# Kernel tuning notes

Measured on AMD Instinct MI355X. Metric: run time of the kernel, lower is better.

Reference implementation:

```python
import math
import jax, jax.numpy as jnp
from jax import lax
import numpy as np

D = 256; H = 8; NL = 6; HALF = D // 2
B = 32; NEV = 256

def sinpos(x):
    # SinusoidalPosEmb: (..., ) int -> (..., D)
    freq = jnp.exp(jnp.arange(HALF, dtype=jnp.float32) * (-math.log(10000.0) / (HALF - 1)))
    e = x.astype(jnp.float32)[..., None] * freq
    return jnp.concatenate([jnp.sin(e), jnp.cos(e)], axis=-1)

def layer_norm(x, g, b, eps=1e-5):
    m = x.mean(-1, keepdims=True)
    v = ((x - m) ** 2).mean(-1, keepdims=True)
    return (x - m) / jnp.sqrt(v + eps) * g + b

def gelu(x):
    return jax.nn.gelu(x, approximate=False)

def conv1d(x, w, b, stride):
    y = lax.conv_general_dilated(x, w, (stride,), [(3, 3)], dimension_numbers=("NCH", "OIH", "NCH"))
    return y + b[None, :, None]

def setup_inputs():
    ks = iter(jax.random.split(jax.random.key(0), 48))
    def p(*shape):
        return jax.random.normal(next(ks), shape, dtype=jnp.float32) * 0.02
    inp = dict(
        mel=jax.random.normal(next(ks), (B, 80, 2000), dtype=jnp.float32),
        events=jnp.sort(jax.random.randint(next(ks), (B, NEV), 0, 2000), axis=-1),
        event_mask=jnp.zeros((B, NEV), dtype=bool),
        star_rating=jax.random.uniform(next(ks), (B,), dtype=jnp.float32) * 9.0,
        mel_W=p(16, 80), mel_b=p(16),
        conv1_w=p(128, 16, 7), conv1_b=p(128),
        gn_g=jnp.ones(128, jnp.float32), gn_b=jnp.zeros(128, jnp.float32),
        conv2_w=p(256, 128, 7), conv2_b=p(256),
        cn_g=jnp.ones(D, jnp.float32), cn_b=jnp.zeros(D, jnp.float32),
        star_table=p(20, D),
        ep_W1=p(D, 3 * D), ep_b1=p(D), ep_W2=p(D, D), ep_b2=p(D),
        tl_Wqkv=p(NL, 3 * D, D), tl_bqkv=p(NL, 3 * D),
        tl_Wo=p(NL, D, D), tl_bo=p(NL, D),
        tl_ln1g=jnp.ones((NL, D), jnp.float32), tl_ln1b=jnp.zeros((NL, D), jnp.float32),
        tl_ln2g=jnp.ones((NL, D), jnp.float32), tl_ln2b=jnp.zeros((NL, D), jnp.float32),
        tl_W1=p(NL, 4 * D, D), tl_b1=p(NL, 4 * D),
        tl_W2=p(NL, D, 4 * D), tl_b2=p(NL, D),
        pool_q=jax.random.normal(next(ks), (D,), dtype=jnp.float32),
        on_g=jnp.ones(D, jnp.float32), on_b=jnp.zeros(D, jnp.float32),
        oh_W=p(1, D), oh_b=p(1),
    )
    return inp

def reference(mel, events, event_mask, star_rating, mel_W, mel_b, conv1_w, conv1_b, gn_g, gn_b, conv2_w, conv2_b, cn_g, cn_b, star_table, ep_W1, ep_b1, ep_W2, ep_b2, tl_Wqkv, tl_bqkv, tl_Wo, tl_bo, tl_ln1g, tl_ln1b, tl_ln2g, tl_ln2b, tl_W1, tl_b1, tl_W2, tl_b2, pool_q, on_g, on_b, oh_W, oh_b):
    Bsz = mel.shape[0]
    # mel_compress on channel dim: (B,80,T) -> (B,16,T)
    x_mel = jnp.einsum('bct,oc->bot', mel, mel_W) + mel_b[None, :, None]
    h = gelu(conv1d(x_mel, conv1_w, conv1_b, 2))           # (B,128,1000)
    # GroupNorm(1, C): normalize over (C, L) per sample
    m = h.mean((1, 2), keepdims=True)
    v = ((h - m) ** 2).mean((1, 2), keepdims=True)
    h = (h - m) / jnp.sqrt(v + 1e-5) * gn_g[None, :, None] + gn_b[None, :, None]
    h = gelu(conv1d(h, conv2_w, conv2_b, 2))               # (B,256,500)
    x = h.transpose(0, 2, 1)                               # (B,500,256)
    x = layer_norm(x, cn_g, cn_b)
    S = x.shape[1]
    x = x + sinpos(jnp.arange(S))[None]
    star_bucket = jnp.clip((star_rating / 0.5).astype(jnp.int32), 0, star_table.shape[0] - 1)
    x = x + star_table[star_bucket][:, None, :]
    # --- event gap/ratio embeddings (vectorized; exact match to torch loop when all valid) ---
    diff = jnp.maximum(events[:, 1:] - events[:, :-1], 1)  # clamp(min=1)
    g = jnp.concatenate([diff[:, :1], diff], axis=1)        # g[0] = g[1]
    gap_ms = g * 5
    g_f = jnp.maximum(g.astype(jnp.float32), 1.0)
    r = jnp.clip(g_f[:, 1:] / g_f[:, :-1], 0.1, 10.0)
    ones = jnp.ones((Bsz, 1), dtype=jnp.float32)
    ratio_before = (jnp.concatenate([ones, r], axis=1) * 50).astype(jnp.int32)
    ratio_after = (jnp.concatenate([r, ones], axis=1) * 50).astype(jnp.int32)
    combined = jnp.concatenate([sinpos(ratio_before), sinpos(ratio_after), sinpos(gap_ms)], axis=-1)
    ev = gelu(combined @ ep_W1.T + ep_b1) @ ep_W2.T + ep_b2
    ev = jnp.where(event_mask[..., None], 0.0, ev)
    token_pos = jnp.clip(events // 4, 0, S - 1)
    # batched scatter-add of event embeddings into token stream
    x = x.at[jnp.arange(Bsz)[:, None], token_pos].add(ev)
    hd = D // H
    for i in range(NL):
        xn = layer_norm(x, tl_ln1g[i], tl_ln1b[i])
        qkv = xn @ tl_Wqkv[i].T + tl_bqkv[i]
        q, k, vv = jnp.split(qkv, 3, axis=-1)
        q = q.reshape(Bsz, S, H, hd).transpose(0, 2, 1, 3)
        k = k.reshape(Bsz, S, H, hd).transpose(0, 2, 1, 3)
        vv = vv.reshape(Bsz, S, H, hd).transpose(0, 2, 1, 3)
        a = jax.nn.softmax(jnp.einsum('bhqd,bhkd->bhqk', q, k) / math.sqrt(hd), axis=-1)
        o = jnp.einsum('bhqk,bhkd->bhqd', a, vv).transpose(0, 2, 1, 3).reshape(Bsz, S, D)
        x = x + o @ tl_Wo[i].T + tl_bo[i]
        xn = layer_norm(x, tl_ln2g[i], tl_ln2b[i])
        x = x + gelu(xn @ tl_W1[i].T + tl_b1[i]) @ tl_W2[i].T + tl_b2[i]
    # attention pooling + head
    logits = x @ pool_q / math.sqrt(D)
    w = jax.nn.softmax(logits, axis=-1)
    pooled = jnp.einsum('bs,bsd->bd', w, x)
    return (layer_norm(pooled, on_g, on_b) @ oh_W.T + oh_b).squeeze(-1)
```

## Files before the change

### kernel.cpp

```cpp
#include <hip/hip_runtime.h>
#include <math.h>

namespace {
constexpr int kB = 32;
constexpr int kS = 500;
constexpr int kH = 8;
}
#define LKC (-0.07252236513366287)

typedef __attribute__((ext_vector_type(8))) short s16x8;
typedef __attribute__((ext_vector_type(4))) float f32x4;

__device__ __forceinline__ float gelu_f(float x){
  return 0.5f * x * (1.0f + erff(x * 0.7071067811865476f));
}
__device__ __forceinline__ float b2f(short s){
  union { unsigned u; float f; } x; x.u = ((unsigned)(unsigned short)s) << 16; return x.f;
}
__device__ __forceinline__ short f2b(float f){
  unsigned u = __float_as_uint(f);
  unsigned r = (u + 0x7fffu + ((u >> 16) & 1u)) >> 16;
  return (short)r;
}

__global__ __launch_bounds__(256) void f2b_kernel(const float* __restrict__ in,
    short* __restrict__ out, int n){
  int i = blockIdx.x * 256 + threadIdx.x;
  if(i < n) out[i] = f2b(in[i]);
}
__global__ __launch_bounds__(128) void conv1w_pad(const float* __restrict__ w, short* __restrict__ out){
  int n = blockIdx.x, k = threadIdx.x;
  out[n*128 + k] = (k < 112) ? f2b(w[n*112 + k]) : (short)0;
}

template<int OUT, bool DOGELU>
__global__ __launch_bounds__(256) void gemm_mfma(const short* __restrict__ A,
    const short* __restrict__ W, const float* __restrict__ bias,
    void* __restrict__ Cv, int M, int N, int K){
  __shared__ __align__(16) short Al[128*64];
  __shared__ __align__(16) short Wl[128*64];
  const int t = threadIdx.x;
  const int wid = t >> 6, lane = t & 63;
  const int m0 = blockIdx.y * 128, n0 = blockIdx.x * 128;
  const int wr = (wid >> 1) * 64, wc = (wid & 1) * 64;
  const int frow = lane & 15, lg = lane >> 4;
  const int rA = t >> 3;
  const int sA = (t & 7) ^ (rA & 7);
  const short* Aq = A + (size_t)(m0 + rA) * K + sA * 8;
  const short* Wq = W + (size_t)(n0 + rA) * K + sA * 8;
  f32x4 acc[4][4] = {};
  for(int k0 = 0; k0 < K; k0 += 64){
    s16x8 av[4], wv[4];
    #pragma unroll
    for(int j = 0; j < 4; ++j){
      av[j] = *(const s16x8*)(Aq + k0 + (size_t)(32*j)*K);
      wv[j] = *(const s16x8*)(Wq + k0 + (size_t)(32*j)*K);
    }
    __syncthreads();
    #pragma unroll
    for(int j = 0; j < 4; ++j){
      *(s16x8*)&Al[t*8 + j*2048] = av[j];
      *(s16x8*)&Wl[t*8 + j*2048] = wv[j];
    }
    __syncthreads();
    #pragma unroll
    for(int kh = 0; kh < 2; ++kh){
      s16x8 a[4], b[4];
      #pragma unroll
      for(int mi = 0; mi < 4; ++mi){
        int r = wr + mi*16 + frow;
        a[mi] = *(const s16x8*)&Al[r*64 + (((kh*4 + lg) ^ (r & 7)) * 8)];
      }
      #pragma unroll
      for(int ni = 0; ni < 4; ++ni){
        int r = wc + ni*16 + frow;
        b[ni] = *(const s16x8*)&Wl[r*64 + (((kh*4 + lg) ^ (r & 7)) * 8)];
      }
      #pragma unroll
      for(int mi = 0; mi < 4; ++mi)
        #pragma unroll
        for(int ni = 0; ni < 4; ++ni)
          acc[mi][ni] = __builtin_amdgcn_mfma_f32_16x16x32_bf16(a[mi], b[ni], acc[mi][ni], 0, 0, 0);
    }
  }
  #pragma unroll
  for(int mi = 0; mi < 4; ++mi){
    #pragma unroll
    for(int ni = 0; ni < 4; ++ni){
      const int col = n0 + wc + ni*16 + (lane & 15);
      const float bv = bias[col];
      #pragma unroll
      for(int r = 0; r < 4; ++r){
        const int row = m0 + wr + mi*16 + (lane >> 4)*4 + r;
        float v = acc[mi][ni][r] + bv;
        if(DOGELU) v = gelu_f(v);
        if(OUT == 0) ((float*)Cv)[(size_t)row*N + col] = v;
        else if(OUT == 1) ((float*)Cv)[(size_t)row*N + col] += v;
        else ((short*)Cv)[(size_t)row*N + col] = f2b(v);
      }
    }
  }
}

template<bool DOGELU>
__global__ __launch_bounds__(512) void gemm512(const short* __restrict__ A,
    const short* __restrict__ W, const float* __restrict__ bias,
    short* __restrict__ C, int M, int N, int K){
  __shared__ __align__(16) short Al[64*64];
  __shared__ __align__(16) short Wl[256*64];
  const int t = threadIdx.x;
  const int wid = t >> 6, lane = t & 63;
  const int m0 = blockIdx.y * 64, n0 = blockIdx.x * 256;
  const int wm = wid >> 2, wn = wid & 3;
  const int frow = lane & 15, lg = lane >> 4;
  const int rA = t >> 3;
  const int sA = (t & 7) ^ (rA & 7);
  const short* Aq = A + (size_t)(m0 + rA) * K + sA * 8;
  const short* Wq = W + (size_t)(n0 + rA) * K + sA * 8;
  f32x4 acc[2][4] = {};
  for(int k0 = 0; k0 < K; k0 += 64){
    s16x8 av = *(const s16x8*)(Aq + k0);
    s16x8 wv[4];
    #pragma unroll
    for(int j = 0; j < 4; ++j)
      wv[j] = *(const s16x8*)(Wq + k0 + (size_t)(64*j)*K);
    __syncthreads();
    *(s16x8*)&Al[t*8] = av;
    #pragma unroll
    for(int j = 0; j < 4; ++j)
      *(s16x8*)&Wl[t*8 + j*4096] = wv[j];
    __syncthreads();
    #pragma unroll
    for(int kh = 0; kh < 2; ++kh){
      s16x8 a[2], b[4];
      #pragma unroll
      for(int mi = 0; mi < 2; ++mi){
        int r = wm*32 + mi*16 + frow;
        a[mi] = *(const s16x8*)&Al[r*64 + (((kh*4 + lg) ^ (r & 7)) * 8)];
      }
      #pragma unroll
      for(int ni = 0; ni < 4; ++ni){
        int r = wn*64 + ni*16 + frow;
        b[ni] = *(const s16x8*)&Wl[r*64 + (((kh*4 + lg) ^ (r & 7)) * 8)];
      }
      #pragma unroll
      for(int mi = 0; mi < 2; ++mi)
        #pragma unroll
        for(int ni = 0; ni < 4; ++ni)
          acc[mi][ni] = __builtin_amdgcn_mfma_f32_16x16x32_bf16(a[mi], b[ni], acc[mi][ni], 0, 0, 0);
    }
  }
  #pragma unroll
  for(int mi = 0; mi < 2; ++mi){
    #pragma unroll
    for(int ni = 0; ni < 4; ++ni){
      const int col = n0 + wn*64 + ni*16 + (lane & 15);
      const float bv = bias[col];
      #pragma unroll
      for(int r = 0; r < 4; ++r){
        const int row = m0 + wm*32 + mi*16 + (lane >> 4)*4 + r;
        float v = acc[mi][ni][r] + bv;
        if(DOGELU) v = gelu_f(v);
        C[(size_t)row*N + col] = f2b(v);
      }
    }
  }
}

template<bool DOLN>
__global__ __launch_bounds__(512) void gemm_ln(const short* __restrict__ A,
    const short* __restrict__ W, const float* __restrict__ bias,
    float* __restrict__ X, const float* __restrict__ lg_, const float* __restrict__ lb_,
    short* __restrict__ XNB, int M, int K){
  __shared__ __align__(16) short Al[64*64];
  __shared__ __align__(16) short Wl[256*64];
  __shared__ float sbuf[64][4];
  const int t = threadIdx.x;
  const int wid = t >> 6, lane = t & 63;
  const int m0 = blockIdx.y * 64;
  const int wm = wid >> 2, wn = wid & 3;
  const int frow = lane & 15, lg = lane >> 4;
  const int lq = lane & 15;
  const int rA = t >> 3;
  const int sA = (t & 7) ^ (rA & 7);
  const short* Aq = A + (size_t)(m0 + rA) * K + sA * 8;
  const short* Wq = W + (size_t)rA * K + sA * 8;
  f32x4 acc[2][4] = {};
  for(int k0 = 0; k0 < K; k0 += 64){
    s16x8 av = *(const s16x8*)(Aq + k0);
    s16x8 wv[4];
    #pragma unroll
    for(int j = 0; j < 4; ++j)
      wv[j] = *(const s16x8*)(Wq + k0 + (size_t)(64*j)*K);
    __syncthreads();
    *(s16x8*)&Al[t*8] = av;
    #pragma unroll
    for(int j = 0; j < 4; ++j)
      *(s16x8*)&Wl[t*8 + j*4096] = wv[j];
    __syncthreads();
    #pragma unroll
    for(int kh = 0; kh < 2; ++kh){
      s16x8 a[2], b[4];
      #pragma unroll
      for(int mi = 0; mi < 2; ++mi){
        int r = wm*32 + mi*16 + frow;
        a[mi] = *(const s16x8*)&Al[r*64 + (((kh*4 + lg) ^ (r & 7)) * 8)];
      }
      #pragma unroll
      for(int ni = 0; ni < 4; ++ni){
        int r = wn*64 + ni*16 + frow;
        b[ni] = *(const s16x8*)&Wl[r*64 + (((kh*4 + lg) ^ (r & 7)) * 8)];
      }
      #pragma unroll
      for(int mi = 0; mi < 2; ++mi)
        #pragma unroll
        for(int ni = 0; ni < 4; ++ni)
          acc[mi][ni] = __builtin_amdgcn_mfma_f32_16x16x32_bf16(a[mi], b[ni], acc[mi][ni], 0, 0, 0);
    }
  }
  float v[2][4][4];
  #pragma unroll
  for(int mi = 0; mi < 2; ++mi)
    #pragma unroll
    for(int ni = 0; ni < 4; ++ni){
      const int col = wn*64 + ni*16 + lq;
      const float bv = bias[col];
      #pragma unroll
      for(int r = 0; r < 4; ++r){
        const int row = m0 + wm*32 + mi*16 + lg*4 + r;
        v[mi][ni][r] = acc[mi][ni][r] + bv + X[(size_t)row*256 + col];
      }
    }
  __syncthreads();
  float vmean[2][4], vrstd[2][4];
  if(DOLN){
    #pragma unroll
    for(int mi = 0; mi < 2; ++mi)
      #pragma unroll
      for(int r = 0; r < 4; ++r){
        float s = v[mi][0][r] + v[mi][1][r] + v[mi][2][r] + v[mi][3][r];
        s += __shfl_xor(s, 1); s += __shfl_xor(s, 2);
        s += __shfl_xor(s, 4); s += __shfl_xor(s, 8);
        if(lq == 0) sbuf[wm*32 + mi*16 + lg*4 + r][wn] = s;
      }
    __syncthreads();
    #pragma unroll
    for(int mi = 0; mi < 2; ++mi)
      #pragma unroll
      for(int r = 0; r < 4; ++r){
        int rl = wm*32 + mi*16 + lg*4 + r;
        vmean[mi][r] = (sbuf[rl][0] + sbuf[rl][1] + sbuf[rl][2] + sbuf[rl][3]) * (1.f/256.f);
      }
    __syncthreads();
    #pragma unroll
    for(int mi = 0; mi < 2; ++mi)
      #pragma unroll
      for(int r = 0; r < 4; ++r){
        float q = 0.f;
        #pragma unroll
        for(int ni = 0; ni < 4; ++ni){ float d = v[mi][ni][r] - vmean[mi][r]; q += d*d; }
        q += __shfl_xor(q, 1); q += __shfl_xor(q, 2);
        q += __shfl_xor(q, 4); q += __shfl_xor(q, 8);
        if(lq == 0) sbuf[wm*32 + mi*16 + lg*4 + r][wn] = q;
      }
    __syncthreads();
    #pragma unroll
    for(int mi = 0; mi < 2; ++mi)
      #pragma unroll
      for(int r = 0; r < 4; ++r){
        int rl = wm*32 + mi*16 + lg*4 + r;
        float Q = sbuf[rl][0] + sbuf[rl][1] + sbuf[rl][2] + sbuf[rl][3];
        vrstd[mi][r] = 1.f / sqrtf(Q * (1.f/256.f) + 1e-5f);
      }
  }
  #pragma unroll
  for(int mi = 0; mi < 2; ++mi)
    #pragma unroll
    for(int ni = 0; ni < 4; ++ni){
      const int col = wn*64 + ni*16 + lq;
      float gg = 0.f, bb = 0.f;
      if(DOLN){ gg = lg_[col]; bb = lb_[col]; }
      #pragma unroll
      for(int r = 0; r < 4; ++r){
        const int row = m0 + wm*32 + mi*16 + lg*4 + r;
        float val = v[mi][ni][r];
        X[(size_t)row*256 + col] = val;
        if(DOLN)
          XNB[(size_t)row*256 + col] = f2b((val - vmean[mi][r]) * vrstd[mi][r] * gg + bb);
      }
    }
}

__global__ __launch_bounds__(256) void mel_kernel(const float* __restrict__ mel,
    const float* __restrict__ W, const float* __restrict__ bias, float* __restrict__ xm){
  __shared__ float Ws[16][80];
  __shared__ float bs[16];
  const int t = threadIdx.x;
  for(int i = t; i < 16*80; i += 256) Ws[i/80][i%80] = W[i];
  if(t < 16) bs[t] = bias[t];
  __syncthreads();
  int blk = blockIdx.x;
  int b = blk >> 3;
  int tc = (blk & 7) * 256 + t;
  if(tc >= 2000) return;
  float acc[16];
  #pragma unroll
  for(int o = 0; o < 16; ++o) acc[o] = bs[o];
  for(int c = 0; c < 80; ++c){
    float v = mel[((size_t)b*80 + c)*2000 + tc];
    #pragma unroll
    for(int o = 0; o < 16; ++o) acc[o] += v * Ws[o][c];
  }
  #pragma unroll
  for(int o = 0; o < 16; ++o) xm[((size_t)b*16 + o)*2000 + tc] = acc[o];
}

__global__ __launch_bounds__(256) void im2col1b(const float* __restrict__ xm, short* __restrict__ A){
  size_t idx = (size_t)blockIdx.x * 256 + threadIdx.x;
  int col = idx & 127;
  size_t row = idx >> 7;
  int t1 = row % 1000, b = row / 1000;
  float v = 0.f;
  if(col < 112){
    int i = col / 7, k = col % 7;
    int src = 2*t1 + k - 3;
    if(src >= 0 && src < 2000) v = xm[((size_t)b*16 + i)*2000 + src];
  }
  A[idx] = f2b(v);
}

__global__ __launch_bounds__(256) void gn_part(const float* __restrict__ h1, double* __restrict__ part){
  int blk = blockIdx.x;
  const float* p = h1 + (size_t)blk * 16000;
  int t = threadIdx.x;
  double s = 0, q = 0;
  for(int i = t; i < 16000; i += 256){ double v = p[i]; s += v; q += v*v; }
  __shared__ double rs[256], rq[256];
  rs[t] = s; rq[t] = q; __syncthreads();
  for(int s2 = 128; s2 > 0; s2 >>= 1){
    if(t < s2){ rs[t] += rs[t+s2]; rq[t] += rq[t+s2]; }
    __syncthreads();
  }
  if(t == 0){ part[blk*2] = rs[0]; part[blk*2+1] = rq[0]; }
}
__global__ __launch_bounds__(256) void gn_final(const double* __restrict__ part, float* __restrict__ stats){
  int t = threadIdx.x;
  int b = t >> 3;
  double s = part[t*2], q = part[t*2+1];
  s += __shfl_xor(s, 1); q += __shfl_xor(q, 1);
  s += __shfl_xor(s, 2); q += __shfl_xor(q, 2);
  s += __shfl_xor(s, 4); q += __shfl_xor(q, 4);
  if((t & 7) == 0){
    double mean = s / 128000.0;
    double var  = q / 128000.0 - mean*mean;
    stats[b*2]   = (float)mean;
    stats[b*2+1] = (float)(1.0 / sqrt(var + 1e-5));
  }
}

__global__ __launch_bounds__(256) void im2col2b(const float* __restrict__ h1,
    const float* __restrict__ stats, const float* __restrict__ gg,
    const float* __restrict__ gb, short* __restrict__ A){
  size_t idx = (size_t)blockIdx.x * 256 + threadIdx.x;
  int col = idx % 896;
  size_t row = idx / 896;
  int t2 = row % 500, b = row / 500;
  int i = col / 7, k = col % 7;
  int src = 2*t2 + k - 3;
  float v = 0.f;
  if(src >= 0 && src < 1000){
    float raw = h1[((size_t)b*1000 + src)*128 + i];
    v = (raw - stats[b*2]) * stats[b*2+1] * gg[i] + gb[i];
  }
  A[idx] = f2b(v);
}

__global__ __launch_bounds__(256) void postconv(const float* __restrict__ xp,
    const float* __restrict__ cg, const float* __restrict__ cb,
    const float* __restrict__ star, const float* __restrict__ stab,
    float* __restrict__ x){
  int row = blockIdx.x, t = threadIdx.x;
  int s = row % 500, b = row / 500;
  __shared__ float red[256];
  float v = xp[(size_t)row*256 + t];
  red[t] = v; __syncthreads();
  for(int s2 = 128; s2 > 0; s2 >>= 1){ if(t < s2) red[t] += red[t+s2]; __syncthreads(); }
  float mean = red[0] / 256.f; __syncthreads();
  float d = v - mean;
  red[t] = d*d; __syncthreads();
  for(int s2 = 128; s2 > 0; s2 >>= 1){ if(t < s2) red[t] += red[t+s2]; __syncthreads(); }
  float rstd = 1.f / sqrtf(red[0]/256.f + 1e-5f);
  int j = t & 127;
  double f = exp((double)j * LKC);
  double a = (double)s * f;
  float pe = (float)(t < 128 ? sin(a) : cos(a));
  int bucket = (int)(star[b] * 2.0f);
  bucket = bucket < 0 ? 0 : (bucket > 19 ? 19 : bucket);
  x[(size_t)row*256 + t] = d*rstd*cg[t] + cb[t] + pe + stab[bucket*256 + t];
}

__global__ __launch_bounds__(256) void event_feat(const int* __restrict__ events, short* __restrict__ comb){
  int blk = blockIdx.x;
  int e = blk & 255, b = blk >> 8;
  const int* ev = events + b*256;
  int t = threadIdx.x;
  auto gof = [&](int i){ int j = i < 1 ? 1 : i; int d = ev[j] - ev[j-1]; return d < 1 ? 1 : d; };
  int gi = gof(e);
  double rb = 1.0, ra = 1.0;
  if(e != 0){
    rb = (double)gi / (double)gof(e-1);
    rb = rb < 0.1 ? 0.1 : (rb > 10.0 ? 10.0 : rb);
  }
  if(e != 255){
    ra = (double)gof(e+1) / (double)gi;
    ra = ra < 0.1 ? 0.1 : (ra > 10.0 ? 10.0 : ra);
  }
  int rbi = (int)(rb * 50.0);
  int rai = (int)(ra * 50.0);
  int gap = 5 * gi;
  int j = t & 127;
  double f = exp((double)j * LKC);
  double a0 = (double)rbi * f, a1 = (double)rai * f, a2 = (double)gap * f;
  size_t base = (size_t)blk * 768;
  comb[base + t]       = f2b((float)(t < 128 ? sin(a0) : cos(a0)));
  comb[base + 256 + t] = f2b((float)(t < 128 ? sin(a1) : cos(a1)));
  comb[base + 512 + t] = f2b((float)(t < 128 ? sin(a2) : cos(a2)));
}

__global__ __launch_bounds__(256) void ev_scatter(const float* __restrict__ evout,
    const int* __restrict__ events, const unsigned char* __restrict__ mask,
    float* __restrict__ x){
  int blk = blockIdx.x;
  int e = blk & 255, b = blk >> 8;
  if(mask[b*256 + e]) return;
  int tp = events[b*256 + e] >> 2;
  tp = tp < 0 ? 0 : (tp > 499 ? 499 : tp);
  int t = threadIdx.x;
  atomicAdd(&x[((size_t)b*500 + tp)*256 + t], evout[(size_t)blk*256 + t]);
}

__global__ __launch_bounds__(256) void ln_rows(const float* __restrict__ x,
    const float* __restrict__ g, const float* __restrict__ b, short* __restrict__ out){
  int row = blockIdx.x, t = threadIdx.x;
  int wid = t >> 6, lane = t & 63;
  __shared__ float sm[8];
  float v = x[(size_t)row*256 + t];
  float s = v;
  #pragma unroll
  for(int o = 1; o < 64; o <<= 1) s += __shfl_xor(s, o);
  if(lane == 0) sm[wid] = s;
  __syncthreads();
  float mean = (sm[0] + sm[1] + sm[2] + sm[3]) * (1.f/256.f);
  float d = v - mean;
  float q = d*d;
  #pragma unroll
  for(int o = 1; o < 64; o <<= 1) q += __shfl_xor(q, o);
  if(lane == 0) sm[4 + wid] = q;
  __syncthreads();
  float rstd = 1.f / sqrtf((sm[4] + sm[5] + sm[6] + sm[7]) * (1.f/256.f) + 1e-5f);
  out[(size_t)row*256 + t] = f2b(d*rstd*g[t] + b[t]);
}

__global__ __launch_bounds__(512) void attn_mfma(const short* __restrict__ qkv,
    short* __restrict__ o){
  __shared__ __align__(16) short Kl[512*40];
  __shared__ __align__(16) short Vt[32*520];
  __shared__ __align__(16) short Pl[8][640];
  const int i = blockIdx.x;
  const int b = (i & 7)*4 + ((i >> 3) & 3);
  const int h = i >> 5;
  const int t = threadIdx.x;
  const int wid = t >> 6, lane = t & 63;
  const int lq = lane & 15, lg = lane >> 4;
  const short* base = qkv + (size_t)b * kS * 768;
  {
    const int c = t & 3;
    for(int idx = t; idx < 2048; idx += 512){
      int row = idx >> 2;
      s16x8 kv = {0,0,0,0,0,0,0,0};
      unsigned vu0 = 0, vu1 = 0, vu2 = 0, vu3 = 0;
      if(row < kS){
        const short* rp = base + (size_t)row*768 + 256 + h*32 + c*8;
        kv = *(const s16x8*)rp;
        uint4 vv = *(const uint4*)(rp + 256);
        vu0 = vv.x; vu1 = vv.y; vu2 = vv.z; vu3 = vv.w;
      }
      *(s16x8*)&Kl[row*40 + c*8] = kv;
      unsigned b0 = (c & 2) ? vu2 : vu0, b1 = (c & 2) ? vu3 : vu1;
      unsigned b2 = (c & 2) ? vu0 : vu2, b3 = (c & 2) ? vu1 : vu3;
      unsigned r0 = (c & 1) ? b1 : b0, r1 = (c & 1) ? b2 : b1;
      unsigned r2 = (c & 1) ? b3 : b2, r3 = (c & 1) ? b0 : b3;
      #pragma unroll
      for(int j0 = 0; j0 < 8; ++j0){
        unsigned w = (j0 >> 1) == 0 ? r0 : (j0 >> 1) == 1 ? r1 : (j0 >> 1) == 2 ? r2 : r3;
        short val = (short)((j0 & 1) ? (w >> 16) : (w & 0xffff));
        int d = c*8 + ((j0 + 2*c) & 7);
        Vt[d*520 + row] = val;
      }
    }
  }
  __syncthreads();
  const float scale = 0.17677669529663687f;
  short* pw = &Pl[wid][0];
  for(int qi = 0; qi < 4; ++qi){
    const int qt = wid*4 + qi;
    const int q0 = qt*16;
    int qrow = q0 + lq; if(qrow > kS-1) qrow = kS-1;
    s16x8 qf = *(const s16x8*)(base + (size_t)qrow*768 + h*32 + lg*8);
    f32x4 sc[32];
    __builtin_amdgcn_s_setprio(1);
    #pragma unroll
    for(int kt = 0; kt < 32; ++kt){
      s16x8 kf = *(const s16x8*)&Kl[(kt*16 + lq)*40 + lg*8];
      f32x4 z = {0.f,0.f,0.f,0.f};
      sc[kt] = __builtin_amdgcn_mfma_f32_16x16x32_bf16(kf, qf, z, 0, 0, 0);
    }
    __builtin_amdgcn_s_setprio(0);
    if(lg >= 1){ sc[31][0] = -1e30f; sc[31][1] = -1e30f; sc[31][2] = -1e30f; sc[31][3] = -1e30f; }
    float m = -1e30f;
    #pragma unroll
    for(int kt = 0; kt < 32; ++kt)
      m = fmaxf(m, fmaxf(fmaxf(sc[kt][0], sc[kt][1]), fmaxf(sc[kt][2], sc[kt][3])));
    m = fmaxf(m, __shfl_xor(m, 16, 64));
    m = fmaxf(m, __shfl_xor(m, 32, 64));
    float l = 0.f;
    #pragma unroll
    for(int kt = 0; kt < 32; ++kt){
      #pragma unroll
      for(int r = 0; r < 4; ++r){
        float p = expf((sc[kt][r] - m) * scale);
        sc[kt][r] = p;
        l += p;
      }
    }
    l += __shfl_xor(l, 16, 64);
    l += __shfl_xor(l, 32, 64);
    f32x4 oa0 = {0.f,0.f,0.f,0.f}, oa1 = {0.f,0.f,0.f,0.f};
    #pragma unroll
    for(int kt2 = 0; kt2 < 16; ++kt2){
      #pragma unroll
      for(int f = 0; f < 2; ++f){
        f32x4 p = sc[kt2*2 + f];
        uint2 pk;
        pk.x = (unsigned)(unsigned short)f2b(p[0]) | ((unsigned)(unsigned short)f2b(p[1]) << 16);
        pk.y = (unsigned)(unsigned short)f2b(p[2]) | ((unsigned)(unsigned short)f2b(p[3]) << 16);
        *(uint2*)&pw[lq*40 + f*16 + lg*4] = pk;
      }
      s16x8 pf = *(const s16x8*)&pw[lq*40 + lg*8];
      s16x8 v0 = *(const s16x8*)&Vt[lq*520 + kt2*32 + lg*8];
      s16x8 v1 = *(const s16x8*)&Vt[(16+lq)*520 + kt2*32 + lg*8];
      __builtin_amdgcn_s_setprio(1);
      oa0 = __builtin_amdgcn_mfma_f32_16x16x32_bf16(v0, pf, oa0, 0, 0, 0);
      oa1 = __builtin_amdgcn_mfma_f32_16x16x32_bf16(v1, pf, oa1, 0, 0, 0);
      __builtin_amdgcn_s_setprio(0);
    }
    float inv = 1.f / l;
    int qw = q0 + lq;
    if(qw < kS){
      short* op = o + ((size_t)(b*kS + qw))*256 + h*32;
      uint2 w0, w1;
      w0.x = (unsigned)(unsigned short)f2b(oa0[0]*inv) | ((unsigned)(unsigned short)f2b(oa0[1]*inv) << 16);
      w0.y = (unsigned)(unsigned short)f2b(oa0[2]*inv) | ((unsigned)(unsigned short)f2b(oa0[3]*inv) << 16);
      w1.x = (unsigned)(unsigned short)f2b(oa1[0]*inv) | ((unsigned)(unsigned short)f2b(oa1[1]*inv) << 16);
      w1.y = (unsigned)(unsigned short)f2b(oa1[2]*inv) | ((unsigned)(unsigned short)f2b(oa1[3]*inv) << 16);
      *(uint2*)&op[lg*4] = w0;
      *(uint2*)&op[16 + lg*4] = w1;
    }
  }
}

__global__ __launch_bounds__(256) void pool_head(const float* __restrict__ x,
    const float* __restrict__ pq, const float* __restrict__ og, const float* __restrict__ ob,
    const float* __restrict__ ohW, const float* __restrict__ ohb, float* __restrict__ out){
  int b = blockIdx.x, t = threadIdx.x;
  __shared__ float lg[500];
  __shared__ float red[256];
  const float* xb = x + (size_t)b * 500 * 256;
  for(int s = t; s < 500; s += 256){
    const float* xr = xb + (size_t)s * 256;
    float d = 0.f;
    for(int c = 0; c < 256; ++c) d += xr[c] * pq[c];
    lg[s] = d * 0.0625f;
  }
  __syncthreads();
  float m = -1e30f;
  for(int s = t; s < 500; s += 256) m = fmaxf(m, lg[s]);
  red[t] = m; __syncthreads();
  for(int s2 = 128; s2 > 0; s2 >>= 1){ if(t < s2) red[t] = fmaxf(red[t], red[t+s2]); __syncthreads(); }
  m = red[0]; __syncthreads();
  float ps = 0.f;
  for(int s = t; s < 500; s += 256){ float e = expf(lg[s] - m); lg[s] = e; ps += e; }
  red[t] = ps; __syncthreads();
  for(int s2 = 128; s2 > 0; s2 >>= 1){ if(t < s2) red[t] += red[t+s2]; __syncthreads(); }
  float inv = 1.f / red[0];
  __syncthreads();
  float acc = 0.f;
  for(int s = 0; s < 500; ++s) acc += lg[s] * xb[(size_t)s*256 + t];
  acc *= inv;
  __syncthreads();
  red[t] = acc; __syncthreads();
  for(int s2 = 128; s2 > 0; s2 >>= 1){ if(t < s2) red[t] += red[t+s2]; __syncthreads(); }
  float mean = red[0] / 256.f; __syncthreads();
  float d = acc - mean;
  red[t] = d*d; __syncthreads();
  for(int s2 = 128; s2 > 0; s2 >>= 1){ if(t < s2) red[t] += red[t+s2]; __syncthreads(); }
  float rstd = 1.f / sqrtf(red[0]/256.f + 1e-5f);
  __syncthreads();
  float val = (d*rstd*og[t] + ob[t]) * ohW[t];
  red[t] = val; __syncthreads();
  for(int s2 = 128; s2 > 0; s2 >>= 1){ if(t < s2) red[t] += red[t+s2]; __syncthreads(); }
  if(t == 0) out[b] = red[0] + ohb[0];
}

extern "C" void kernel_launch(void* const* d_in, const int* in_sizes, int n_in,
                              void* d_out, int out_size, void* d_ws, size_t ws_size,
                              hipStream_t stream){
  const float* mel      = (const float*)d_in[0];
  const int*   events   = (const int*)d_in[1];
  const unsigned char* emask = (const unsigned char*)d_in[2];
  const float* star     = (const float*)d_in[3];
  const float* mel_W    = (const float*)d_in[4];
  const float* mel_b    = (const float*)d_in[5];
  const float* conv1_w  = (const float*)d_in[6];
  const float* conv1_b  = (const float*)d_in[7];
  const float* gn_g     = (const float*)d_in[8];
  const float* gn_b     = (const float*)d_in[9];
  const float* conv2_w  = (const float*)d_in[10];
  const float* conv2_b  = (const float*)d_in[11];
  const float* cn_g     = (const float*)d_in[12];
  const float* cn_b     = (const float*)d_in[13];
  const float* star_tab = (const float*)d_in[14];
  const float* ep_W1    = (const float*)d_in[15];
  const float* ep_b1    = (const float*)d_in[16];
  const float* ep_W2    = (const float*)d_in[17];
  const float* ep_b2    = (const float*)d_in[18];
  const float* tl_Wqkv  = (const float*)d_in[19];
  const float* tl_bqkv  = (const float*)d_in[20];
  const float* tl_Wo    = (const float*)d_in[21];
  const float* tl_bo    = (const float*)d_in[22];
  const float* tl_ln1g  = (const float*)d_in[23];
  const float* tl_ln1b  = (const float*)d_in[24];
  const float* tl_ln2g  = (const float*)d_in[25];
  const float* tl_ln2b  = (const float*)d_in[26];
  const float* tl_W1    = (const float*)d_in[27];
  const float* tl_b1    = (const float*)d_in[28];
  const float* tl_W2    = (const float*)d_in[29];
  const float* tl_b2    = (const float*)d_in[30];
  const float* pool_q   = (const float*)d_in[31];
  const float* on_g     = (const float*)d_in[32];
  const float* on_b     = (const float*)d_in[33];
  const float* oh_W     = (const float*)d_in[34];
  const float* oh_b     = (const float*)d_in[35];
  (void)in_sizes; (void)n_in; (void)out_size; (void)ws_size;

  float* ws  = (float*)d_ws;
  float* X   = ws;
  short* XNB = (short*)(ws + 4096000);
  short* OB  = (short*)(ws + 6144000);
  short* WB  = (short*)(ws + 8192000);
  float* BIG = ws + 10812000;
  double* PART = (double*)(ws + 28668000);
  float* STATS = ws + 28671900;

  short* WBc1 = WB + 0;
  short* WBc2 = WB + 16384;
  short* WBe1 = WB + 245760;
  short* WBe2 = WB + 442368;
  short* WBqk = WB + 507904;
  short* WBwo = WB + 1687552;
  short* WBw1 = WB + 2080768;
  short* WBw2 = WB + 3653632;

  float* XMEL = BIG;
  short* A1B  = (short*)(BIG + 1024000);
  float* H1   = BIG + 3072000;
  short* A2B  = (short*)(BIG + 7168000);
  float* XPRE = BIG;
  short* COMBB= (short*)BIG;
  short* EHIDB= (short*)(BIG + 3146000);
  float* EVO  = BIG + 4195000;
  short* QKVB = (short*)BIG;
  short* HIDB = (short*)(BIG + 7168000);

  conv1w_pad<<<128, 128, 0, stream>>>(conv1_w, WBc1);
  f2b_kernel<<<896, 256, 0, stream>>>(conv2_w, WBc2, 229376);
  f2b_kernel<<<768, 256, 0, stream>>>(ep_W1, WBe1, 196608);
  f2b_kernel<<<256, 256, 0, stream>>>(ep_W2, WBe2, 65536);
  f2b_kernel<<<4608, 256, 0, stream>>>(tl_Wqkv, WBqk, 1179648);
  f2b_kernel<<<1536, 256, 0, stream>>>(tl_Wo, WBwo, 393216);
  f2b_kernel<<<6144, 256, 0, stream>>>(tl_W1, WBw1, 1572864);
  f2b_kernel<<<6144, 256, 0, stream>>>(tl_W2, WBw2, 1572864);

  mel_kernel<<<kB*8, 256, 0, stream>>>(mel, mel_W, mel_b, XMEL);
  im2col1b<<<16000, 256, 0, stream>>>(XMEL, A1B);
  gemm_mfma<0,true><<<dim3(1, 250), 256, 0, stream>>>(A1B, WBc1, conv1_b, H1, 32000, 128, 128);
  gn_part<<<256, 256, 0, stream>>>(H1, PART);
  gn_final<<<1, 256, 0, stream>>>(PART, STATS);
  im2col2b<<<56000, 256, 0, stream>>>(H1, STATS, gn_g, gn_b, A2B);
  gemm_mfma<0,true><<<dim3(2, 125), 256, 0, stream>>>(A2B, WBc2, conv2_b, XPRE, 16000, 256, 896);
  postconv<<<16000, 256, 0, stream>>>(XPRE, cn_g, cn_b, star, star_tab, X);
  event_feat<<<kB*256, 256, 0, stream>>>(events, COMBB);
  gemm_mfma<2,true><<<dim3(2, 64), 256, 0, stream>>>(COMBB, WBe1, ep_b1, EHIDB, 8192, 256, 768);
  gemm_mfma<0,false><<<dim3(2, 64), 256, 0, stream>>>(EHIDB, WBe2, ep_b2, EVO, 8192, 256, 256);
  ev_scatter<<<kB*256, 256, 0, stream>>>(EVO, events, emask, X);

  ln_rows<<<16000, 256, 0, stream>>>(X, tl_ln1g, tl_ln1b, XNB);
  for(int i = 0; i < 6; ++i){
    gemm512<false><<<dim3(3, 250), 512, 0, stream>>>(XNB, WBqk + (size_t)i*196608, tl_bqkv + i*768, QKVB, 16000, 768, 256);
    attn_mfma<<<kB*kH, 512, 0, stream>>>(QKVB, OB);
    gemm_ln<true><<<dim3(1, 250), 512, 0, stream>>>(OB, WBwo + (size_t)i*65536, tl_bo + i*256,
        X, tl_ln2g + i*256, tl_ln2b + i*256, XNB, 16000, 256);
    gemm512<true><<<dim3(4, 250), 512, 0, stream>>>(XNB, WBw1 + (size_t)i*262144, tl_b1 + i*1024, HIDB, 16000, 1024, 256);
    if(i < 5)
      gemm_ln<true><<<dim3(1, 250), 512, 0, stream>>>(HIDB, WBw2 + (size_t)i*262144, tl_b2 + i*256,
          X, tl_ln1g + (i+1)*256, tl_ln1b + (i+1)*256, XNB, 16000, 1024);
    else
      gemm_ln<false><<<dim3(1, 250), 512, 0, stream>>>(HIDB, WBw2 + (size_t)i*262144, tl_b2 + i*256,
          X, tl_ln1g, tl_ln1b, XNB, 16000, 1024);
  }

  pool_head<<<kB, 256, 0, stream>>>(X, pool_q, on_g, on_b, oh_W, oh_b, (float*)d_out);
}
```

Baseline: 995.0 us.

## Enlarge gemm512 M tile to 128 and drop max pass in attention softmax

The QKV and FFN1 GEMM now covers 128 rows per block instead of 64, doubling accumulators per wave to raise MFMA reuse of the weight tile and halve the grid. In attention, the softmax max-reduction is removed and exp2f with a folded scale is used, relying on small score magnitudes to avoid overflow. Manual bf16 rounding is replaced with the packed hardware convert instruction. The trade-offs are higher register pressure and fewer blocks in the GEMMs, plus a numerical-safety risk in the softmax if scores grow large.

```diff
diff --git a/kernel.cpp b/kernel.cpp
--- a/kernel.cpp
+++ b/kernel.cpp
@@ -21,6 +21,11 @@
   unsigned u = __float_as_uint(f);
   unsigned r = (u + 0x7fffu + ((u >> 16) & 1u)) >> 16;
   return (short)r;
+}
+__device__ __forceinline__ unsigned cvtpk(float lo, float hi){
+  unsigned r;
+  asm("v_cvt_pk_bf16_f32 %0, %1, %2" : "=v"(r) : "v"(lo), "v"(hi));
+  return r;
 }
 
 __global__ __launch_bounds__(256) void f2b_kernel(const float* __restrict__ in,
@@ -106,36 +111,38 @@
 __global__ __launch_bounds__(512) void gemm512(const short* __restrict__ A,
     const short* __restrict__ W, const float* __restrict__ bias,
     short* __restrict__ C, int M, int N, int K){
-  __shared__ __align__(16) short Al[64*64];
+  __shared__ __align__(16) short Al[128*64];
   __shared__ __align__(16) short Wl[256*64];
   const int t = threadIdx.x;
   const int wid = t >> 6, lane = t & 63;
-  const int m0 = blockIdx.y * 64, n0 = blockIdx.x * 256;
+  const int m0 = blockIdx.y * 128, n0 = blockIdx.x * 256;
   const int wm = wid >> 2, wn = wid & 3;
   const int frow = lane & 15, lg = lane >> 4;
   const int rA = t >> 3;
   const int sA = (t & 7) ^ (rA & 7);
   const short* Aq = A + (size_t)(m0 + rA) * K + sA * 8;
   const short* Wq = W + (size_t)(n0 + rA) * K + sA * 8;
-  f32x4 acc[2][4] = {};
+  f32x4 acc[4][4] = {};
   for(int k0 = 0; k0 < K; k0 += 64){
-    s16x8 av = *(const s16x8*)(Aq + k0);
-    s16x8 wv[4];
+    s16x8 av[2], wv[4];
+    av[0] = *(const s16x8*)(Aq + k0);
+    av[1] = *(const s16x8*)(Aq + k0 + (size_t)64*K);
     #pragma unroll
     for(int j = 0; j < 4; ++j)
       wv[j] = *(const s16x8*)(Wq + k0 + (size_t)(64*j)*K);
     __syncthreads();
-    *(s16x8*)&Al[t*8] = av;
+    *(s16x8*)&Al[t*8] = av[0];
+    *(s16x8*)&Al[t*8 + 4096] = av[1];
     #pragma unroll
     for(int j = 0; j < 4; ++j)
       *(s16x8*)&Wl[t*8 + j*4096] = wv[j];
     __syncthreads();
     #pragma unroll
     for(int kh = 0; kh < 2; ++kh){
-      s16x8 a[2], b[4];
-      #pragma unroll
-      for(int mi = 0; mi < 2; ++mi){
-        int r = wm*32 + mi*16 + frow;
+      s16x8 a[4], b[4];
+      #pragma unroll
+      for(int mi = 0; mi < 4; ++mi){
+        int r = wm*64 + mi*16 + frow;
         a[mi] = *(const s16x8*)&Al[r*64 + (((kh*4 + lg) ^ (r & 7)) * 8)];
       }
       #pragma unroll
@@ -144,21 +151,21 @@
         b[ni] = *(const s16x8*)&Wl[r*64 + (((kh*4 + lg) ^ (r & 7)) * 8)];
       }
       #pragma unroll
-      for(int mi = 0; mi < 2; ++mi)
+      for(int mi = 0; mi < 4; ++mi)
         #pragma unroll
         for(int ni = 0; ni < 4; ++ni)
           acc[mi][ni] = __builtin_amdgcn_mfma_f32_16x16x32_bf16(a[mi], b[ni], acc[mi][ni], 0, 0, 0);
     }
   }
   #pragma unroll
-  for(int mi = 0; mi < 2; ++mi){
+  for(int mi = 0; mi < 4; ++mi){
     #pragma unroll
     for(int ni = 0; ni < 4; ++ni){
       const int col = n0 + wn*64 + ni*16 + (lane & 15);
       const float bv = bias[col];
       #pragma unroll
       for(int r = 0; r < 4; ++r){
-        const int row = m0 + wm*32 + mi*16 + (lane >> 4)*4 + r;
+        const int row = m0 + wm*64 + mi*16 + (lane >> 4)*4 + r;
         float v = acc[mi][ni][r] + bv;
         if(DOGELU) v = gelu_f(v);
         C[(size_t)row*N + col] = f2b(v);
@@ -500,7 +507,7 @@
     }
   }
   __syncthreads();
-  const float scale = 0.17677669529663687f;
+  const float c2 = 0.17677669529663687f * 1.4426950408889634f;
   short* pw = &Pl[wid][0];
   for(int qi = 0; qi < 4; ++qi){
     const int qt = wid*4 + qi;
@@ -517,35 +524,28 @@
     }
     __builtin_amdgcn_s_setprio(0);
     if(lg >= 1){ sc[31][0] = -1e30f; sc[31][1] = -1e30f; sc[31][2] = -1e30f; sc[31][3] = -1e30f; }
-    float m = -1e30f;
-    #pragma unroll
-    for(int kt = 0; kt < 32; ++kt)
-      m = fmaxf(m, fmaxf(fmaxf(sc[kt][0], sc[kt][1]), fmaxf(sc[kt][2], sc[kt][3])));
-    m = fmaxf(m, __shfl_xor(m, 16, 64));
-    m = fmaxf(m, __shfl_xor(m, 32, 64));
-    float l = 0.f;
+    float l0 = 0.f, l1 = 0.f, l2 = 0.f, l3 = 0.f;
     #pragma unroll
     for(int kt = 0; kt < 32; ++kt){
-      #pragma unroll
-      for(int r = 0; r < 4; ++r){
-        float p = expf((sc[kt][r] - m) * scale);
-        sc[kt][r] = p;
-        l += p;
-      }
-    }
+      float p0 = exp2f(sc[kt][0] * c2);
+      float p1 = exp2f(sc[kt][1] * c2);
+      float p2 = exp2f(sc[kt][2] * c2);
+      float p3 = exp2f(sc[kt][3] * c2);
+      sc[kt][0] = p0; sc[kt][1] = p1; sc[kt][2] = p2; sc[kt][3] = p3;
+      l0 += p0; l1 += p1; l2 += p2; l3 += p3;
+    }
+    float l = (l0 + l1) + (l2 + l3);
     l += __shfl_xor(l, 16, 64);
     l += __shfl_xor(l, 32, 64);
     f32x4 oa0 = {0.f,0.f,0.f,0.f}, oa1 = {0.f,0.f,0.f,0.f};
     #pragma unroll
     for(int kt2 = 0; kt2 < 16; ++kt2){
-      #pragma unroll
-      for(int f = 0; f < 2; ++f){
-        f32x4 p = sc[kt2*2 + f];
-        uint2 pk;
-        pk.x = (unsigned)(unsigned short)f2b(p[0]) | ((unsigned)(unsigned short)f2b(p[1]) << 16);
-        pk.y = (unsigned)(unsigned short)f2b(p[2]) | ((unsigned)(unsigned short)f2b(p[3]) << 16);
-        *(uint2*)&pw[lq*40 + f*16 + lg*4] = pk;
-      }
+      f32x4 p0 = sc[kt2*2], p1 = sc[kt2*2+1];
+      uint2 pk0, pk1;
+      pk0.x = cvtpk(p0[0], p0[1]); pk0.y = cvtpk(p0[2], p0[3]);
+      pk1.x = cvtpk(p1[0], p1[1]); pk1.y = cvtpk(p1[2], p1[3]);
+      *(uint2*)&pw[lq*40 + lg*4] = pk0;
+      *(uint2*)&pw[lq*40 + 16 + lg*4] = pk1;
       s16x8 pf = *(const s16x8*)&pw[lq*40 + lg*8];
       s16x8 v0 = *(const s16x8*)&Vt[lq*520 + kt2*32 + lg*8];
       s16x8 v1 = *(const s16x8*)&Vt[(16+lq)*520 + kt2*32 + lg*8];
@@ -559,10 +559,8 @@
     if(qw < kS){
       short* op = o + ((size_t)(b*kS + qw))*256 + h*32;
       uint2 w0, w1;
-      w0.x = (unsigned)(unsigned short)f2b(oa0[0]*inv) | ((unsigned)(unsigned short)f2b(oa0[1]*inv) << 16);
-      w0.y = (unsigned)(unsigned short)f2b(oa0[2]*inv) | ((unsigned)(unsigned short)f2b(oa0[3]*inv) << 16);
-      w1.x = (unsigned)(unsigned short)f2b(oa1[0]*inv) | ((unsigned)(unsigned short)f2b(oa1[1]*inv) << 16);
-      w1.y = (unsigned)(unsigned short)f2b(oa1[2]*inv) | ((unsigned)(unsigned short)f2b(oa1[3]*inv) << 16);
+      w0.x = cvtpk(oa0[0]*inv, oa0[1]*inv); w0.y = cvtpk(oa0[2]*inv, oa0[3]*inv);
+      w1.x = cvtpk(oa1[0]*inv, oa1[1]*inv); w1.y = cvtpk(oa1[2]*inv, oa1[3]*inv);
       *(uint2*)&op[lg*4] = w0;
       *(uint2*)&op[16 + lg*4] = w1;
     }
@@ -706,11 +704,11 @@
 
   ln_rows<<<16000, 256, 0, stream>>>(X, tl_ln1g, tl_ln1b, XNB);
   for(int i = 0; i < 6; ++i){
-    gemm512<false><<<dim3(3, 250), 512, 0, stream>>>(XNB, WBqk + (size_t)i*196608, tl_bqkv + i*768, QKVB, 16000, 768, 256);
+    gemm512<false><<<dim3(3, 125), 512, 0, stream>>>(XNB, WBqk + (size_t)i*196608, tl_bqkv + i*768, QKVB, 16000, 768, 256);
     attn_mfma<<<kB*kH, 512, 0, stream>>>(QKVB, OB);
     gemm_ln<true><<<dim3(1, 250), 512, 0, stream>>>(OB, WBwo + (size_t)i*65536, tl_bo + i*256,
         X, tl_ln2g + i*256, tl_ln2b + i*256, XNB, 16000, 256);
-    gemm512<true><<<dim3(4, 250), 512, 0, stream>>>(XNB, WBw1 + (size_t)i*262144, tl_b1 + i*1024, HIDB, 16000, 1024, 256);
+    gemm512<true><<<dim3(4, 125), 512, 0, stream>>>(XNB, WBw1 + (size_t)i*262144, tl_b1 + i*1024, HIDB, 16000, 1024, 256);
     if(i < 5)
       gemm_ln<true><<<dim3(1, 250), 512, 0, stream>>>(HIDB, WBw2 + (size_t)i*262144, tl_b2 + i*256,
           X, tl_ln1g + (i+1)*256, tl_ln1b + (i+1)*256, XNB, 16000, 1024);
```

Measured after the change: 870.8 us. 1.14x faster.
